# Optimization experiments

Measured on AMD Instinct MI355X. Metric: run time of the kernel, lower is better.

The kernel has to match this reference:

```python
import jax, jax.numpy as jnp
import numpy as np

TAU = 10.0
N, D = 4096, 8192  # batch, feature dim (D >= N required by the original indexing)
NUM_CLASSES = 100


def setup_inputs() -> dict:
    key = jax.random.key(0)
    k1, k2 = jax.random.split(key)
    embeddings = jax.random.normal(k1, (N, D), dtype=jnp.float32)
    labels = jax.random.randint(k2, (N,), 0, NUM_CLASSES, dtype=jnp.int64)
    return {"embeddings": embeddings, "labels": labels}


def reference(embeddings, labels):
    # Faithful to the original (buggy) torch math:
    # inner_product[i, d] = exp(emb[i, d]**2 / tau)  (trailing singleton dim dropped)
    n = embeddings.shape[0]
    A = jnp.exp(embeddings * embeddings / TAU)          # [N, D]
    # denominator_i = sum_d A[i, d] - A[i, i]
    denom = jnp.sum(A, axis=1) - jnp.diagonal(A)[:n]    # [N]
    # numerator terms: exp(A[i, j] / tau) for j in batch indices (j < N <= D)
    B = jnp.exp(A[:, :n] / TAU)                          # [N, N]
    same = labels[:, None] == labels[None, :]            # [N, N]
    mask = same & ~jnp.eye(n, dtype=bool)
    counts = jnp.sum(mask, axis=1).astype(embeddings.dtype)   # misma_clase per i
    suma = jnp.sum(jnp.where(mask, B, jnp.zeros((), B.dtype)), axis=1) / denom  # [N]
    return jnp.sum(jnp.log(suma / counts))
```

## Files before the change

kernel.cpp:

```cpp
#include <hip/hip_runtime.h>

static constexpr int N = 4096;
static constexpr int D = 8192;
static constexpr int BLOCK = 256;

__global__ __launch_bounds__(BLOCK) void supcon_partial(
    const float* __restrict__ emb,
    const int* __restrict__ labels,
    float4* __restrict__ wsA,
    float* __restrict__ wsB)
{
    const int wave = threadIdx.x >> 6;
    const int lane = threadIdx.x & 63;
    const int waveId = blockIdx.x * 4 + wave;
    const int row = waveId >> 2;
    const int q   = waveId & 3;

    const float4* rowp = reinterpret_cast<const float4*>(emb + (size_t)row * D);

    if (q < 2) {
        const int lab_i = labels[row];
        const int4* labp = reinterpret_cast<const int4*>(labels);
        float4 v[8]; int4 lj[8];
        #pragma unroll
        for (int i = 0; i < 8; ++i) {
            const int idx = q * 512 + i * 64 + lane;
            v[i]  = rowp[idx];
            lj[i] = labp[idx];
        }
        __builtin_amdgcn_sched_barrier(0);
        float denom = 0.f, ssum = 0.f, fcnt = 0.f, diag = 0.f;
        #pragma unroll
        for (int i = 0; i < 8; ++i) {
            const int j0 = (q * 512 + i * 64 + lane) * 4;
            const float xs[4] = {v[i].x, v[i].y, v[i].z, v[i].w};
            const int   ls[4] = {lj[i].x, lj[i].y, lj[i].z, lj[i].w};
            #pragma unroll
            for (int k = 0; k < 4; ++k) {
                float a = __expf(xs[k] * xs[k] * 0.1f);
                denom += a;
                float b = __expf(a * 0.1f);
                bool m = (ls[k] == lab_i);
                ssum += m ? b : 0.f;
                fcnt += m ? 1.f : 0.f;
                diag += (j0 + k == row) ? a : 0.f;
            }
        }
        #pragma unroll
        for (int off = 32; off > 0; off >>= 1) {
            denom += __shfl_down(denom, off);
            ssum  += __shfl_down(ssum,  off);
            fcnt  += __shfl_down(fcnt,  off);
            diag  += __shfl_down(diag,  off);
        }
        if (lane == 0)
            wsA[row * 2 + q] = make_float4(denom, ssum, fcnt, diag);
    } else {
        float4 v[8];
        #pragma unroll
        for (int i = 0; i < 8; ++i)
            v[i] = rowp[1024 + (q - 2) * 512 + i * 64 + lane];
        __builtin_amdgcn_sched_barrier(0);
        float denom = 0.f;
        #pragma unroll
        for (int i = 0; i < 8; ++i) {
            denom += __expf(v[i].x * v[i].x * 0.1f);
            denom += __expf(v[i].y * v[i].y * 0.1f);
            denom += __expf(v[i].z * v[i].z * 0.1f);
            denom += __expf(v[i].w * v[i].w * 0.1f);
        }
        #pragma unroll
        for (int off = 32; off > 0; off >>= 1)
            denom += __shfl_down(denom, off);
        if (lane == 0)
            wsB[row * 2 + (q - 2)] = denom;
    }
}

__global__ __launch_bounds__(256) void supcon_combine(
    const float4* __restrict__ wsA,
    const float* __restrict__ wsB,
    float* __restrict__ out)
{
    const int row = blockIdx.x * 256 + threadIdx.x;
    const float4 p0 = wsA[row * 2 + 0];
    const float4 p1 = wsA[row * 2 + 1];
    const float b0 = wsB[row * 2 + 0];
    const float b1 = wsB[row * 2 + 1];
    const float ad = p0.w + p1.w;

    const float denom = (p0.x + p1.x + b0 + b1) - ad;
    const float ssum  = (p0.y + p1.y) - __expf(ad * 0.1f);
    const float fcnt  = (p0.z + p1.z) - 1.f;
    float val = __logf(ssum) - __logf(denom) - __logf(fcnt);

    #pragma unroll
    for (int off = 32; off > 0; off >>= 1)
        val += __shfl_down(val, off);
    __shared__ float sb[4];
    if ((threadIdx.x & 63) == 0) sb[threadIdx.x >> 6] = val;
    __syncthreads();
    if (threadIdx.x == 0)
        atomicAdd(out, sb[0] + sb[1] + sb[2] + sb[3]);
}

extern "C" void kernel_launch(void* const* d_in, const int* in_sizes, int n_in,
                              void* d_out, int out_size, void* d_ws, size_t ws_size,
                              hipStream_t stream) {
    const float* emb  = (const float*)d_in[0];
    const int* labels = (const int*)d_in[1];
    float* out        = (float*)d_out;

    float4* wsA = (float4*)d_ws;
    float*  wsB = (float*)((char*)d_ws + N * 2 * sizeof(float4));

    hipMemsetAsync(out, 0, sizeof(float), stream);
    supcon_partial<<<dim3(N), dim3(BLOCK), 0, stream>>>(emb, labels, wsA, wsB);
    supcon_combine<<<dim3(N / 256), dim3(256), 0, stream>>>(wsA, wsB, out);
}
```

Measured before the change: 188.0 us.

## Software-pipeline row loads, raise occupancy, single-block combine without memset

```diff
diff --git a/kernel.cpp b/kernel.cpp
--- a/kernel.cpp
+++ b/kernel.cpp
@@ -4,7 +4,7 @@
 static constexpr int D = 8192;
 static constexpr int BLOCK = 256;
 
-__global__ __launch_bounds__(BLOCK) void supcon_partial(
+__global__ __launch_bounds__(BLOCK, 6) void supcon_partial(
     const float* __restrict__ emb,
     const int* __restrict__ labels,
     float4* __restrict__ wsA,
@@ -21,30 +21,52 @@
     if (q < 2) {
         const int lab_i = labels[row];
         const int4* labp = reinterpret_cast<const int4*>(labels);
-        float4 v[8]; int4 lj[8];
-        #pragma unroll
-        for (int i = 0; i < 8; ++i) {
-            const int idx = q * 512 + i * 64 + lane;
-            v[i]  = rowp[idx];
-            lj[i] = labp[idx];
-        }
-        __builtin_amdgcn_sched_barrier(0);
+        const int base = q * 512 + lane;
+
+        float4 a0 = rowp[base], a1 = rowp[base + 64];
+        int4   l0 = labp[base], l1 = labp[base + 64];
+
         float denom = 0.f, ssum = 0.f, fcnt = 0.f, diag = 0.f;
         #pragma unroll
-        for (int i = 0; i < 8; ++i) {
-            const int j0 = (q * 512 + i * 64 + lane) * 4;
-            const float xs[4] = {v[i].x, v[i].y, v[i].z, v[i].w};
-            const int   ls[4] = {lj[i].x, lj[i].y, lj[i].z, lj[i].w};
-            #pragma unroll
-            for (int k = 0; k < 4; ++k) {
-                float a = __expf(xs[k] * xs[k] * 0.1f);
-                denom += a;
-                float b = __expf(a * 0.1f);
-                bool m = (ls[k] == lab_i);
-                ssum += m ? b : 0.f;
-                fcnt += m ? 1.f : 0.f;
-                diag += (j0 + k == row) ? a : 0.f;
+        for (int c = 0; c < 4; ++c) {
+            float4 b0 = {}, b1 = {}; int4 m0 = {}, m1 = {};
+            if (c < 3) {
+                const int nb = base + (c + 1) * 128;
+                b0 = rowp[nb]; b1 = rowp[nb + 64];
+                m0 = labp[nb]; m1 = labp[nb + 64];
             }
+            __builtin_amdgcn_sched_barrier(0);
+            {
+                const int j0 = (base + c * 128) * 4;
+                const float xs[4] = {a0.x, a0.y, a0.z, a0.w};
+                const int   ls[4] = {l0.x, l0.y, l0.z, l0.w};
+                #pragma unroll
+                for (int k = 0; k < 4; ++k) {
+                    float a = __expf(xs[k] * xs[k] * 0.1f);
+                    denom += a;
+                    float b = __expf(a * 0.1f);
+                    bool m = (ls[k] == lab_i);
+                    ssum += m ? b : 0.f;
+                    fcnt += m ? 1.f : 0.f;
+                    diag += (j0 + k == row) ? a : 0.f;
+                }
+            }
+            {
+                const int j0 = (base + c * 128 + 64) * 4;
+                const float xs[4] = {a1.x, a1.y, a1.z, a1.w};
+                const int   ls[4] = {l1.x, l1.y, l1.z, l1.w};
+                #pragma unroll
+                for (int k = 0; k < 4; ++k) {
+                    float a = __expf(xs[k] * xs[k] * 0.1f);
+                    denom += a;
+                    float b = __expf(a * 0.1f);
+                    bool m = (ls[k] == lab_i);
+                    ssum += m ? b : 0.f;
+                    fcnt += m ? 1.f : 0.f;
+                    diag += (j0 + k == row) ? a : 0.f;
+                }
+            }
+            a0 = b0; a1 = b1; l0 = m0; l1 = m1;
         }
         #pragma unroll
         for (int off = 32; off > 0; off >>= 1) {
@@ -56,18 +78,26 @@
         if (lane == 0)
             wsA[row * 2 + q] = make_float4(denom, ssum, fcnt, diag);
     } else {
-        float4 v[8];
-        #pragma unroll
-        for (int i = 0; i < 8; ++i)
-            v[i] = rowp[1024 + (q - 2) * 512 + i * 64 + lane];
-        __builtin_amdgcn_sched_barrier(0);
+        const int base = 1024 + (q - 2) * 512 + lane;
+        float4 a0 = rowp[base], a1 = rowp[base + 64];
         float denom = 0.f;
         #pragma unroll
-        for (int i = 0; i < 8; ++i) {
-            denom += __expf(v[i].x * v[i].x * 0.1f);
-            denom += __expf(v[i].y * v[i].y * 0.1f);
-            denom += __expf(v[i].z * v[i].z * 0.1f);
-            denom += __expf(v[i].w * v[i].w * 0.1f);
+        for (int c = 0; c < 4; ++c) {
+            float4 b0 = {}, b1 = {};
+            if (c < 3) {
+                const int nb = base + (c + 1) * 128;
+                b0 = rowp[nb]; b1 = rowp[nb + 64];
+            }
+            __builtin_amdgcn_sched_barrier(0);
+            denom += __expf(a0.x * a0.x * 0.1f);
+            denom += __expf(a0.y * a0.y * 0.1f);
+            denom += __expf(a0.z * a0.z * 0.1f);
+            denom += __expf(a0.w * a0.w * 0.1f);
+            denom += __expf(a1.x * a1.x * 0.1f);
+            denom += __expf(a1.y * a1.y * 0.1f);
+            denom += __expf(a1.z * a1.z * 0.1f);
+            denom += __expf(a1.w * a1.w * 0.1f);
+            a0 = b0; a1 = b1;
         }
         #pragma unroll
         for (int off = 32; off > 0; off >>= 1)
@@ -77,31 +107,38 @@
     }
 }
 
-__global__ __launch_bounds__(256) void supcon_combine(
+__global__ __launch_bounds__(1024) void supcon_combine(
     const float4* __restrict__ wsA,
     const float* __restrict__ wsB,
     float* __restrict__ out)
 {
-    const int row = blockIdx.x * 256 + threadIdx.x;
-    const float4 p0 = wsA[row * 2 + 0];
-    const float4 p1 = wsA[row * 2 + 1];
-    const float b0 = wsB[row * 2 + 0];
-    const float b1 = wsB[row * 2 + 1];
-    const float ad = p0.w + p1.w;
-
-    const float denom = (p0.x + p1.x + b0 + b1) - ad;
-    const float ssum  = (p0.y + p1.y) - __expf(ad * 0.1f);
-    const float fcnt  = (p0.z + p1.z) - 1.f;
-    float val = __logf(ssum) - __logf(denom) - __logf(fcnt);
-
+    const int tid = threadIdx.x;
+    float val = 0.f;
+    #pragma unroll
+    for (int k = 0; k < 4; ++k) {
+        const int row = tid + k * 1024;
+        const float4 p0 = wsA[row * 2 + 0];
+        const float4 p1 = wsA[row * 2 + 1];
+        const float b0 = wsB[row * 2 + 0];
+        const float b1 = wsB[row * 2 + 1];
+        const float ad = p0.w + p1.w;
+        const float denom = (p0.x + p1.x + b0 + b1) - ad;
+        const float ssum  = (p0.y + p1.y) - __expf(ad * 0.1f);
+        const float fcnt  = (p0.z + p1.z) - 1.f;
+        val += __logf(ssum) - __logf(denom) - __logf(fcnt);
+    }
     #pragma unroll
     for (int off = 32; off > 0; off >>= 1)
         val += __shfl_down(val, off);
-    __shared__ float sb[4];
-    if ((threadIdx.x & 63) == 0) sb[threadIdx.x >> 6] = val;
+    __shared__ float sb[16];
+    if ((tid & 63) == 0) sb[tid >> 6] = val;
     __syncthreads();
-    if (threadIdx.x == 0)
-        atomicAdd(out, sb[0] + sb[1] + sb[2] + sb[3]);
+    if (tid == 0) {
+        float t = 0.f;
+        #pragma unroll
+        for (int w = 0; w < 16; ++w) t += sb[w];
+        *out = t;
+    }
 }
 
 extern "C" void kernel_launch(void* const* d_in, const int* in_sizes, int n_in,
@@ -114,7 +151,6 @@
     float4* wsA = (float4*)d_ws;
     float*  wsB = (float*)((char*)d_ws + N * 2 * sizeof(float4));
 
-    hipMemsetAsync(out, 0, sizeof(float), stream);
     supcon_partial<<<dim3(N), dim3(BLOCK), 0, stream>>>(emb, labels, wsA, wsB);
-    supcon_combine<<<dim3(N / 256), dim3(256), 0, stream>>>(wsA, wsB, out);
+    supcon_combine<<<dim3(1), dim3(1024), 0, stream>>>(wsA, wsB, out);
 }
```

Measured after the change: 189.2 us. About the same (+0.6%).
